# Kernel optimization log

Measured on AMD Instinct MI355X. Metric: run time of the kernel, lower is better.

## Reference

```python
import jax, jax.numpy as jnp
import numpy as np

B, C, IC, H = 16, 256, 64, 56
EPS = 1e-5
SCALE = float((H * H * C) ** -0.5)


def conv1x1(x, w, b=None):
    # x: [B,Cin,H,W], w: [Cout,Cin]
    y = jnp.einsum('bchw,oc->bohw', x, w)
    return y if b is None else y + b[None, :, None, None]


def bn_eval(x, g, be):
    # eval-mode BatchNorm2d with running_mean=0, running_var=1
    s = g / np.float32(np.sqrt(1.0 + EPS))
    return x * s[None, :, None, None] + be[None, :, None, None]


def lrelu(x):
    return jnp.where(x >= 0, x, 0.2 * x)


def setup_inputs() -> dict:
    key = jax.random.key(0)
    ks = jax.random.split(key, 16)
    def w(i, shape, s=0.05):
        return jax.random.normal(ks[i], shape, jnp.float32) * s
    return {
        'x_s': w(0, (B, C, H, H), 1.0),
        'x_fq': w(1, (B, C, H, H), 1.0),
        'x_mt': w(2, (B, C, H, H), 1.0),
        # local_att: conv(C->IC)+BN+LReLU+conv(IC->C)+BN
        'la_w1': w(3, (IC, C)), 'la_b1': jnp.zeros(IC, jnp.float32),
        'la_g1': jnp.ones(IC, jnp.float32), 'la_be1': jnp.zeros(IC, jnp.float32),
        'la_w2': w(4, (C, IC)), 'la_b2': jnp.zeros(C, jnp.float32),
        'la_g2': jnp.ones(C, jnp.float32), 'la_be2': jnp.zeros(C, jnp.float32),
        'lk_w': w(5, (C, C)), 'lk_b': jnp.zeros(C, jnp.float32),
        'lv_w': w(6, (C, C)),  # l_convv has bias=False
        # global_att (after avg-pool): conv+BN+LReLU+conv+BN
        'ga_w1': w(7, (IC, C)), 'ga_b1': jnp.zeros(IC, jnp.float32),
        'ga_g1': jnp.ones(IC, jnp.float32), 'ga_be1': jnp.zeros(IC, jnp.float32),
        'ga_w2': w(8, (C, IC)), 'ga_b2': jnp.zeros(C, jnp.float32),
        'ga_g2': jnp.ones(C, jnp.float32), 'ga_be2': jnp.zeros(C, jnp.float32),
        'gk_w': w(9, (C, C)), 'gk_b': jnp.zeros(C, jnp.float32),
        'gv_w': w(10, (C, C)),  # convv has bias=False
        'c11_w': w(11, (C, C)), 'c11_b': jnp.zeros(C, jnp.float32),
        'c1_w': w(12, (C, C)), 'c1_b': jnp.zeros(C, jnp.float32),
    }


def reference(x_s, x_fq, x_mt,
              la_w1, la_b1, la_g1, la_be1, la_w2, la_b2, la_g2, la_be2,
              lk_w, lk_b, lv_w,
              ga_w1, ga_b1, ga_g1, ga_be1, ga_w2, ga_b2, ga_g2, ga_be2,
              gk_w, gk_b, gv_w, c11_w, c11_b, c1_w, c1_b):
    # ---- local branch ----
    l_q = bn_eval(conv1x1(lrelu(bn_eval(conv1x1(x_s, la_w1, la_b1), la_g1, la_be1)),
                          la_w2, la_b2), la_g2, la_be2)
    l_k = conv1x1(x_s, lk_w, lk_b)
    l_v = conv1x1(x_s, lv_w)
    # l_q @ l_k^T over the spatial matrix of each (b,c): [H,W]@[W,H]->[H,H]
    att = jax.nn.softmax(jnp.einsum('bchw,bcvw->bchv', l_q, l_k) * SCALE, axis=-1)
    l_fuse = jnp.einsum('bchv,bcvw->bchw', att, l_v)  # [B,C,H,W]
    # ---- global branch ----
    p = jnp.mean(conv1x1(x_mt, c11_w, c11_b), axis=(2, 3), keepdims=True)  # [B,C,1,1]
    g_q = bn_eval(conv1x1(lrelu(bn_eval(conv1x1(p, ga_w1, ga_b1), ga_g1, ga_be1)),
                          ga_w2, ga_b2), ga_g2, ga_be2)  # [B,C,1,1]
    g_k = conv1x1(x_fq, gk_w, gk_b)
    g_v = conv1x1(x_fq, gv_w)
    gatt = jax.nn.softmax(g_q * g_k * SCALE, axis=-1)  # softmax over W
    g_fuse = jnp.einsum('bchk,bckw->bchw', gatt, g_v)  # requires H==W (square maps)
    # ---- output conv: kernel 1 with padding 1 -> spatial grows to H+2 ----
    f = jnp.pad(l_fuse + g_fuse, ((0, 0), (0, 0), (1, 1), (1, 1)))
    return conv1x1(f, c1_w, c1_b)  # [B,C,H+2,W+2]
```

## Files before the change

kernel.cpp:

```cpp
#include <hip/hip_runtime.h>
#include <hip/hip_bf16.h>

typedef __bf16 bf16;
typedef __bf16 bf16x8 __attribute__((ext_vector_type(8)));
typedef float  f32x4  __attribute__((ext_vector_type(4)));

#define S_SP 3136
#define SCALE_V (1.0f/896.0f)

__device__ __forceinline__ float bf2f(bf16 x) { return (float)x; }

__device__ __forceinline__ bf16x8 load8(const float* p) {
    f32x4 a = *(const f32x4*)p;
    f32x4 b = *(const f32x4*)(p + 4);
    bf16x8 r;
    r[0] = (bf16)a[0]; r[1] = (bf16)a[1]; r[2] = (bf16)a[2]; r[3] = (bf16)a[3];
    r[4] = (bf16)b[0]; r[5] = (bf16)b[1]; r[6] = (bf16)b[2]; r[7] = (bf16)b[3];
    return r;
}
__device__ __forceinline__ bf16x8 load8(const bf16* p) { return *(const bf16x8*)p; }

__global__ __launch_bounds__(256)
void conv_multi_kernel(const float* __restrict__ X,
                       const float* __restrict__ Wa, const float* __restrict__ ba,
                       bf16* __restrict__ Ya,
                       const float* __restrict__ Wb, bf16* __restrict__ Yb,
                       const float* __restrict__ Wc, const float* __restrict__ bc,
                       const float* __restrict__ gc, const float* __restrict__ bec,
                       bf16* __restrict__ Yc)
{
    __shared__ bf16 Xt[64][72];
    const int s0  = blockIdx.x * 64;
    const int sec = blockIdx.y;
    const int b   = blockIdx.z;
    const int tid = threadIdx.x;
    const int wv = tid >> 6, lane = tid & 63, li = lane & 15, quad = lane >> 4;

    const float* Xb = X + (size_t)b * 256 * S_SP;

    const float* W; const float* bias = nullptr;
    const float* bng = nullptr; const float* bnb = nullptr;
    bf16* Y; int o0, O; bool two, lrelu = false;
    if (sec < 2)      { W = Wa; bias = ba; Y = Ya; o0 = sec * 128;       two = true;  O = 256; }
    else if (sec < 4) { W = Wb;            Y = Yb; o0 = (sec - 2) * 128; two = true;  O = 256; }
    else              { W = Wc; bias = bc; bng = gc; bnb = bec; Y = Yc;
                        o0 = 0; two = false; lrelu = true; O = 64; }

    f32x4 acc[2][4];
    #pragma unroll
    for (int mt = 0; mt < 2; ++mt)
        #pragma unroll
        for (int nt = 0; nt < 4; ++nt) acc[mt][nt] = f32x4{0.f, 0.f, 0.f, 0.f};

    #pragma unroll
    for (int k0 = 0; k0 < 256; k0 += 32) {
        if (k0) __syncthreads();
        {
            int cl  = tid >> 3;
            int sj  = (tid & 7) * 8;
            int g   = cl >> 3;
            int clo = cl & 7;
            bf16x8 v = load8(Xb + (size_t)(k0 + cl) * S_SP + s0 + sj);
            #pragma unroll
            for (int u = 0; u < 8; ++u) {
                int r  = sj + u;
                int gp = g ^ ((r >> 3) & 3);
                Xt[r][gp * 8 + clo] = v[u];
            }
        }
        __syncthreads();
        bf16x8 a0 = load8(W + (size_t)(o0 + wv * 16 + li) * 256 + k0 + quad * 8);
        bf16x8 a1;
        if (two) a1 = load8(W + (size_t)(o0 + 64 + wv * 16 + li) * 256 + k0 + quad * 8);
        #pragma unroll
        for (int nt = 0; nt < 4; ++nt) {
            int row = nt * 16 + li;
            int gp  = quad ^ ((row >> 3) & 3);
            bf16x8 bb = *(const bf16x8*)&Xt[row][gp * 8];
            acc[0][nt] = __builtin_amdgcn_mfma_f32_16x16x32_bf16(a0, bb, acc[0][nt], 0, 0, 0);
            if (two)
                acc[1][nt] = __builtin_amdgcn_mfma_f32_16x16x32_bf16(a1, bb, acc[1][nt], 0, 0, 0);
        }
    }

    const float rs = rsqrtf(1.0f + 1e-5f);
    const int nm = two ? 2 : 1;
    for (int mt = 0; mt < nm; ++mt) {
        #pragma unroll
        for (int r = 0; r < 4; ++r) {
            int o = o0 + mt * 64 + wv * 16 + quad * 4 + r;
            float bi = bias ? bias[o] : 0.f;
            float sc = bng ? bng[o] * rs : 1.f;
            float sh = bnb ? bnb[o] : 0.f;
            #pragma unroll
            for (int nt = 0; nt < 4; ++nt) {
                float v = acc[mt][nt][r] + bi;
                v = v * sc + sh;
                if (lrelu) v = (v >= 0.f) ? v : 0.2f * v;
                int s = s0 + nt * 16 + li;
                Y[((size_t)b * O + o) * S_SP + s] = (bf16)v;
            }
        }
    }
}

template<typename TX, typename TY, int CIN, int MT, bool LRELU, bool PAD_OUT>
__global__ __launch_bounds__(256)
void conv1x1_kernel(const TX* __restrict__ X, const float* __restrict__ W,
                    const float* __restrict__ bias, const float* __restrict__ bng,
                    const float* __restrict__ bnb, TY* __restrict__ Y, int O)
{
    __shared__ bf16 Xt[64][72];
    const int s0  = blockIdx.x * 64;
    const int o0  = blockIdx.y * (MT * 64);
    const int b   = blockIdx.z;
    const int tid = threadIdx.x;
    const int wv = tid >> 6, lane = tid & 63, li = lane & 15, quad = lane >> 4;

    const TX* Xb = X + (size_t)b * CIN * S_SP;

    f32x4 acc[MT][4];
    #pragma unroll
    for (int mt = 0; mt < MT; ++mt)
        #pragma unroll
        for (int nt = 0; nt < 4; ++nt) acc[mt][nt] = f32x4{0.f, 0.f, 0.f, 0.f};

    #pragma unroll
    for (int k0 = 0; k0 < CIN; k0 += 32) {
        if (k0) __syncthreads();
        {
            int cl  = tid >> 3;
            int sj  = (tid & 7) * 8;
            int g   = cl >> 3;
            int clo = cl & 7;
            bf16x8 v = load8(Xb + (size_t)(k0 + cl) * S_SP + s0 + sj);
            #pragma unroll
            for (int u = 0; u < 8; ++u) {
                int r  = sj + u;
                int gp = g ^ ((r >> 3) & 3);
                Xt[r][gp * 8 + clo] = v[u];
            }
        }
        __syncthreads();
        bf16x8 a[MT];
        #pragma unroll
        for (int mt = 0; mt < MT; ++mt)
            a[mt] = load8(W + (size_t)(o0 + mt * 64 + wv * 16 + li) * CIN + k0 + quad * 8);
        #pragma unroll
        for (int nt = 0; nt < 4; ++nt) {
            int row = nt * 16 + li;
            int gp  = quad ^ ((row >> 3) & 3);
            bf16x8 bb = *(const bf16x8*)&Xt[row][gp * 8];
            #pragma unroll
            for (int mt = 0; mt < MT; ++mt)
                acc[mt][nt] = __builtin_amdgcn_mfma_f32_16x16x32_bf16(a[mt], bb, acc[mt][nt], 0, 0, 0);
        }
    }

    const float rs = rsqrtf(1.0f + 1e-5f);
    #pragma unroll
    for (int mt = 0; mt < MT; ++mt) {
        #pragma unroll
        for (int r = 0; r < 4; ++r) {
            int o = o0 + mt * 64 + wv * 16 + quad * 4 + r;
            float bi = bias ? bias[o] : 0.f;
            float sc = bng ? bng[o] * rs : 1.f;
            float sh = bnb ? bnb[o] : 0.f;
            #pragma unroll
            for (int nt = 0; nt < 4; ++nt) {
                float v = acc[mt][nt][r] + bi;
                v = v * sc + sh;
                if (LRELU) v = (v >= 0.f) ? v : 0.2f * v;
                int s = s0 + nt * 16 + li;
                if (!PAD_OUT) {
                    Y[((size_t)b * O + o) * S_SP + s] = (TY)v;
                } else {
                    int rr = s / 56, cc = s % 56;
                    Y[(((size_t)b * O + o) * 58 + rr + 1) * 58 + cc + 1] = (TY)v;
                }
            }
        }
    }
}

__global__ __launch_bounds__(256)
void attn_kernel(const bf16* __restrict__ Q, const bf16* __restrict__ K,
                 const bf16* __restrict__ V, const float* __restrict__ gq,
                 const bf16* __restrict__ GK, const bf16* __restrict__ GV,
                 bf16* __restrict__ F)
{
    __shared__ bf16 Qs[64][72], Ks[64][72], Vt[64][72], Ps[64][72];
    const int bc  = blockIdx.x;
    const int tid = threadIdx.x;
    const int wv = tid >> 6, lane = tid & 63, li = lane & 15, quad = lane >> 4;
    const int m0 = wv * 16;

    #pragma unroll
    for (int i = tid; i < 64 * 36; i += 256) {
        ((uint32_t*)Qs)[i] = 0; ((uint32_t*)Ks)[i] = 0;
        ((uint32_t*)Vt)[i] = 0; ((uint32_t*)Ps)[i] = 0;
    }
    __syncthreads();

    const bf16* Qp = Q + (size_t)bc * S_SP;
    const bf16* Kp = K + (size_t)bc * S_SP;
    const bf16* Vp = V + (size_t)bc * S_SP;
    for (int idx = tid; idx < 392; idx += 256) {
        int r = idx / 7, cj = (idx % 7) * 8;
        *(bf16x8*)&Qs[r][cj] = *(const bf16x8*)(Qp + r * 56 + cj);
        *(bf16x8*)&Ks[r][cj] = *(const bf16x8*)(Kp + r * 56 + cj);
        bf16x8 vv = *(const bf16x8*)(Vp + r * 56 + cj);
        int q = r >> 3, rlo = r & 7;
        #pragma unroll
        for (int u = 0; u < 8; ++u) {
            int row = cj + u;
            int gp  = q ^ ((row >> 3) & 3);
            Vt[row][gp * 8 + rlo] = vv[u];
        }
    }

    const float gs = gq[bc];
    const bf16* GVp = GV + (size_t)bc * S_SP;
    const bf16* GKp = GK + (size_t)bc * S_SP;
    const int ra  = tid / 7,            cja = (tid % 7) * 8;
    const bool hasb = tid < 136;
    const int rb  = (tid + 256) / 7,    cjb = ((tid + 256) % 7) * 8;
    bf16x8 gva = *(const bf16x8*)(GVp + ra * 56 + cja);
    bf16x8 gvb = hasb ? *(const bf16x8*)(GVp + rb * 56 + cjb) : bf16x8{};
    __syncthreads();

    f32x4 sacc[4];
    #pragma unroll
    for (int nt = 0; nt < 4; ++nt) sacc[nt] = f32x4{0.f, 0.f, 0.f, 0.f};
    #pragma unroll
    for (int k0 = 0; k0 < 64; k0 += 32) {
        bf16x8 a = *(const bf16x8*)&Qs[m0 + li][k0 + quad * 8];
        #pragma unroll
        for (int nt = 0; nt < 4; ++nt) {
            bf16x8 bb = *(const bf16x8*)&Ks[nt * 16 + li][k0 + quad * 8];
            sacc[nt] = __builtin_amdgcn_mfma_f32_16x16x32_bf16(a, bb, sacc[nt], 0, 0, 0);
        }
    }

    #pragma unroll
    for (int r = 0; r < 4; ++r) {
        float e[4]; float m = -3e38f;
        #pragma unroll
        for (int nt = 0; nt < 4; ++nt) {
            int v = nt * 16 + li;
            float x = (v < 56) ? sacc[nt][r] * SCALE_V : -3e38f;
            e[nt] = x; m = fmaxf(m, x);
        }
        m = fmaxf(m, __shfl_xor(m, 1)); m = fmaxf(m, __shfl_xor(m, 2));
        m = fmaxf(m, __shfl_xor(m, 4)); m = fmaxf(m, __shfl_xor(m, 8));
        float s = 0.f;
        #pragma unroll
        for (int nt = 0; nt < 4; ++nt) {
            float p = (nt * 16 + li < 56) ? __expf(e[nt] - m) : 0.f;
            e[nt] = p; s += p;
        }
        s += __shfl_xor(s, 1); s += __shfl_xor(s, 2);
        s += __shfl_xor(s, 4); s += __shfl_xor(s, 8);
        float inv = 1.f / s;
        int row = m0 + quad * 4 + r;
        #pragma unroll
        for (int nt = 0; nt < 4; ++nt) Ps[row][nt * 16 + li] = (bf16)(e[nt] * inv);
    }

    float gkv[4][4];
    #pragma unroll
    for (int r = 0; r < 4; ++r) {
        int row = m0 + quad * 4 + r;
        int hrow = (row < 56) ? row : 0;
        #pragma unroll
        for (int nt = 0; nt < 4; ++nt) {
            int v = nt * 16 + li;
            gkv[r][nt] = (v < 56) ? bf2f(GKp[hrow * 56 + v]) : 0.f;
        }
    }
    __syncthreads();

    f32x4 oacc[4];
    #pragma unroll
    for (int nt = 0; nt < 4; ++nt) oacc[nt] = f32x4{0.f, 0.f, 0.f, 0.f};
    #pragma unroll
    for (int k0 = 0; k0 < 64; k0 += 32) {
        bf16x8 a = *(const bf16x8*)&Ps[m0 + li][k0 + quad * 8];
        int kq = (k0 >> 3) + quad;
        #pragma unroll
        for (int nt = 0; nt < 4; ++nt) {
            int row = nt * 16 + li;
            int gp  = kq ^ ((row >> 3) & 3);
            bf16x8 bb = *(const bf16x8*)&Vt[row][gp * 8];
            oacc[nt] = __builtin_amdgcn_mfma_f32_16x16x32_bf16(a, bb, oacc[nt], 0, 0, 0);
        }
    }

    __syncthreads();

    {
        int q = ra >> 3, rlo = ra & 7;
        #pragma unroll
        for (int u = 0; u < 8; ++u) {
            int row = cja + u;
            int gp  = q ^ ((row >> 3) & 3);
            Vt[row][gp * 8 + rlo] = gva[u];
        }
        if (hasb) {
            int qb = rb >> 3, rblo = rb & 7;
            #pragma unroll
            for (int u = 0; u < 8; ++u) {
                int row = cjb + u;
                int gp  = qb ^ ((row >> 3) & 3);
                Vt[row][gp * 8 + rblo] = gvb[u];
            }
        }
    }

    #pragma unroll
    for (int r = 0; r < 4; ++r) {
        float e[4]; float m = -3e38f;
        #pragma unroll
        for (int nt = 0; nt < 4; ++nt) {
            int v = nt * 16 + li;
            float x = (v < 56) ? gs * gkv[r][nt] : -3e38f;
            e[nt] = x; m = fmaxf(m, x);
        }
        m = fmaxf(m, __shfl_xor(m, 1)); m = fmaxf(m, __shfl_xor(m, 2));
        m = fmaxf(m, __shfl_xor(m, 4)); m = fmaxf(m, __shfl_xor(m, 8));
        float s = 0.f;
        #pragma unroll
        for (int nt = 0; nt < 4; ++nt) {
            float p = (nt * 16 + li < 56) ? __expf(e[nt] - m) : 0.f;
            e[nt] = p; s += p;
        }
        s += __shfl_xor(s, 1); s += __shfl_xor(s, 2);
        s += __shfl_xor(s, 4); s += __shfl_xor(s, 8);
        float inv = 1.f / s;
        int row = m0 + quad * 4 + r;
        #pragma unroll
        for (int nt = 0; nt < 4; ++nt) Ps[row][nt * 16 + li] = (bf16)(e[nt] * inv);
    }
    __syncthreads();

    #pragma unroll
    for (int k0 = 0; k0 < 64; k0 += 32) {
        bf16x8 a = *(const bf16x8*)&Ps[m0 + li][k0 + quad * 8];
        int kq = (k0 >> 3) + quad;
        #pragma unroll
        for (int nt = 0; nt < 4; ++nt) {
            int row = nt * 16 + li;
            int gp  = kq ^ ((row >> 3) & 3);
            bf16x8 bb = *(const bf16x8*)&Vt[row][gp * 8];
            oacc[nt] = __builtin_amdgcn_mfma_f32_16x16x32_bf16(a, bb, oacc[nt], 0, 0, 0);
        }
    }

    bf16* Fp = F + (size_t)bc * S_SP;
    #pragma unroll
    for (int r = 0; r < 4; ++r) {
        int h = m0 + quad * 4 + r;
        #pragma unroll
        for (int nt = 0; nt < 4; ++nt) {
            int w = nt * 16 + li;
            if (h < 56 && w < 56) Fp[h * 56 + w] = (bf16)oacc[nt][r];
        }
    }
}

__global__ __launch_bounds__(256)
void spatial_mean_kernel(const float* __restrict__ X, float* __restrict__ out)
{
    int bc = blockIdx.x, tid = threadIdx.x;
    const float* p = X + (size_t)bc * S_SP;
    float s = 0.f;
    for (int i = tid; i < S_SP; i += 256) s += p[i];
    for (int off = 32; off; off >>= 1) s += __shfl_down(s, off, 64);
    __shared__ float ws[4];
    if ((tid & 63) == 0) ws[tid >> 6] = s;
    __syncthreads();
    if (tid == 0) out[bc] = (ws[0] + ws[1] + ws[2] + ws[3]) * (1.0f / S_SP);
}

__global__ __launch_bounds__(256)
void gq_kernel(const float* __restrict__ pmean,
               const float* c11w, const float* c11b,
               const float* gaw1, const float* gab1, const float* gag1, const float* gabe1,
               const float* gaw2, const float* gab2, const float* gag2, const float* gabe2,
               float* __restrict__ gq)
{
    __shared__ float pm[256], p2[256], hh[64];
    int b = blockIdx.x, t = threadIdx.x;
    pm[t] = pmean[b * 256 + t];
    __syncthreads();
    float a = c11b[t];
    for (int c = 0; c < 256; ++c) a += c11w[t * 256 + c] * pm[c];
    p2[t] = a;
    __syncthreads();
    const float rs = rsqrtf(1.0f + 1e-5f);
    if (t < 64) {
        float h = gab1[t];
        for (int c = 0; c < 256; ++c) h += gaw1[t * 256 + c] * p2[c];
        h = h * (gag1[t] * rs) + gabe1[t];
        hh[t] = (h >= 0.f) ? h : 0.2f * h;
    }
    __syncthreads();
    float g = gab2[t];
    for (int i = 0; i < 64; ++i) g += gaw2[t * 64 + i] * hh[i];
    g = g * (gag2[t] * rs) + gabe2[t];
    gq[b * 256 + t] = g * SCALE_V;
}

__global__ __launch_bounds__(256)
void fill_border_kernel(float* __restrict__ out, const float* __restrict__ c1b)
{
    int idx = blockIdx.x * 256 + threadIdx.x;
    int e  = idx % 228;
    int bo = idx / 228;
    if (bo >= 16 * 256) return;
    int o = bo & 255;
    int r, c;
    if (e < 58)       { r = 0;  c = e; }
    else if (e < 116) { r = 57; c = e - 58; }
    else { int t = e - 116; r = 1 + (t >> 1); c = (t & 1) * 57; }
    out[(size_t)bo * 3364 + r * 58 + c] = c1b[o];
}

extern "C" void kernel_launch(void* const* d_in, const int* in_sizes, int n_in,
                              void* d_out, int out_size, void* d_ws, size_t ws_size,
                              hipStream_t stream)
{
    (void)in_sizes; (void)n_in; (void)out_size; (void)ws_size;
    const float* x_s   = (const float*)d_in[0];
    const float* x_fq  = (const float*)d_in[1];
    const float* x_mt  = (const float*)d_in[2];
    const float* la_w1 = (const float*)d_in[3];
    const float* la_b1 = (const float*)d_in[4];
    const float* la_g1 = (const float*)d_in[5];
    const float* la_be1= (const float*)d_in[6];
    const float* la_w2 = (const float*)d_in[7];
    const float* la_b2 = (const float*)d_in[8];
    const float* la_g2 = (const float*)d_in[9];
    const float* la_be2= (const float*)d_in[10];
    const float* lk_w  = (const float*)d_in[11];
    const float* lk_b  = (const float*)d_in[12];
    const float* lv_w  = (const float*)d_in[13];
    const float* ga_w1 = (const float*)d_in[14];
    const float* ga_b1 = (const float*)d_in[15];
    const float* ga_g1 = (const float*)d_in[16];
    const float* ga_be1= (const float*)d_in[17];
    const float* ga_w2 = (const float*)d_in[18];
    const float* ga_b2 = (const float*)d_in[19];
    const float* ga_g2 = (const float*)d_in[20];
    const float* ga_be2= (const float*)d_in[21];
    const float* gk_w  = (const float*)d_in[22];
    const float* gk_b  = (const float*)d_in[23];
    const float* gv_w  = (const float*)d_in[24];
    const float* c11_w = (const float*)d_in[25];
    const float* c11_b = (const float*)d_in[26];
    const float* c1_w  = (const float*)d_in[27];
    const float* c1_b  = (const float*)d_in[28];
    float* out = (float*)d_out;

    char* ws = (char*)d_ws;
    const size_t SZ = (size_t)16 * 256 * S_SP * 2;
    bf16* Q  = (bf16*)(ws);
    bf16* K  = (bf16*)(ws + SZ);
    bf16* V  = (bf16*)(ws + 2 * SZ);
    bf16* GK = (bf16*)(ws + 3 * SZ);
    bf16* GV = (bf16*)(ws + 4 * SZ);
    bf16* Hd = (bf16*)(ws + 5 * SZ);
    float* pmean = (float*)(ws + 5 * SZ + (size_t)16 * 64 * S_SP * 2);
    float* gq    = pmean + 16 * 256;
    bf16* F  = Q;

    dim3 blk(256);
    fill_border_kernel<<<dim3(3648), blk, 0, stream>>>(out, c1_b);

    conv_multi_kernel<<<dim3(49, 5, 16), blk, 0, stream>>>(
        x_s, lk_w, lk_b, K, lv_w, V,
        la_w1, la_b1, la_g1, la_be1, Hd);
    conv1x1_kernel<bf16, bf16, 64, 2, false, false><<<dim3(49, 2, 16), blk, 0, stream>>>(
        Hd, la_w2, la_b2, la_g2, la_be2, Q, 256);

    spatial_mean_kernel<<<dim3(4096), blk, 0, stream>>>(x_mt, pmean);
    gq_kernel<<<dim3(16), blk, 0, stream>>>(pmean, c11_w, c11_b,
        ga_w1, ga_b1, ga_g1, ga_be1, ga_w2, ga_b2, ga_g2, ga_be2, gq);
    conv_multi_kernel<<<dim3(49, 4, 16), blk, 0, stream>>>(
        x_fq, gk_w, gk_b, GK, gv_w, GV,
        nullptr, nullptr, nullptr, nullptr, nullptr);

    attn_kernel<<<dim3(4096), blk, 0, stream>>>(Q, K, V, gq, GK, GV, F);

    conv1x1_kernel<bf16, float, 256, 2, false, true><<<dim3(49, 2, 16), blk, 0, stream>>>(
        F, c1_w, c1_b, nullptr, nullptr, out, 256);
}
```

Baseline: 508.4 us.

## Double-buffer conv input tiles and remap workgroups so XCDs share input tiles

```diff
diff --git a/kernel.cpp b/kernel.cpp
--- a/kernel.cpp
+++ b/kernel.cpp
@@ -20,6 +20,21 @@
 }
 __device__ __forceinline__ bf16x8 load8(const bf16* p) { return *(const bf16x8*)p; }
 
+template<typename T> struct raw8;
+template<> struct raw8<float> { f32x4 a, b; };
+template<> struct raw8<bf16>  { bf16x8 v; };
+__device__ __forceinline__ raw8<float> loadraw(const float* p) {
+    return { *(const f32x4*)p, *(const f32x4*)(p + 4) };
+}
+__device__ __forceinline__ raw8<bf16> loadraw(const bf16* p) {
+    return { *(const bf16x8*)p };
+}
+__device__ __forceinline__ bf16 elem8(const raw8<float>& r, int u) {
+    return (bf16)(u < 4 ? r.a[u] : r.b[u - 4]);
+}
+__device__ __forceinline__ bf16 elem8(const raw8<bf16>& r, int u) { return r.v[u]; }
+
+template<int NSEC>
 __global__ __launch_bounds__(256)
 void conv_multi_kernel(const float* __restrict__ X,
                        const float* __restrict__ Wa, const float* __restrict__ ba,
@@ -29,10 +44,15 @@
                        const float* __restrict__ gc, const float* __restrict__ bec,
                        bf16* __restrict__ Yc)
 {
-    __shared__ bf16 Xt[64][72];
-    const int s0  = blockIdx.x * 64;
-    const int sec = blockIdx.y;
-    const int b   = blockIdx.z;
+    __shared__ bf16 Xt[2][64][72];
+    const int wg  = blockIdx.x;
+    const int xcd = wg & 7;
+    const int idx = wg >> 3;
+    const int sec = idx % NSEC;
+    const int t   = idx / NSEC;
+    const int tile = xcd * 98 + t;
+    const int s0  = (tile % 49) * 64;
+    const int b   = tile / 49;
     const int tid = threadIdx.x;
     const int wv = tid >> 6, lane = tid & 63, li = lane & 15, quad = lane >> 4;
 
@@ -52,22 +72,24 @@
         #pragma unroll
         for (int nt = 0; nt < 4; ++nt) acc[mt][nt] = f32x4{0.f, 0.f, 0.f, 0.f};
 
+    const int cl  = tid >> 3;
+    const int sj  = (tid & 7) * 8;
+    const int g   = cl >> 3;
+    const int clo = cl & 7;
+    const float* xp = Xb + (size_t)cl * S_SP + s0 + sj;
+
+    raw8<float> v = loadraw(xp);
+    int p = 0;
     #pragma unroll
     for (int k0 = 0; k0 < 256; k0 += 32) {
-        if (k0) __syncthreads();
-        {
-            int cl  = tid >> 3;
-            int sj  = (tid & 7) * 8;
-            int g   = cl >> 3;
-            int clo = cl & 7;
-            bf16x8 v = load8(Xb + (size_t)(k0 + cl) * S_SP + s0 + sj);
-            #pragma unroll
-            for (int u = 0; u < 8; ++u) {
-                int r  = sj + u;
-                int gp = g ^ ((r >> 3) & 3);
-                Xt[r][gp * 8 + clo] = v[u];
-            }
-        }
+        #pragma unroll
+        for (int u = 0; u < 8; ++u) {
+            int r  = sj + u;
+            int gp = g ^ ((r >> 3) & 3);
+            Xt[p][r][gp * 8 + clo] = elem8(v, u);
+        }
+        raw8<float> vn = v;
+        if (k0 + 32 < 256) vn = loadraw(xp + (size_t)(k0 + 32) * S_SP);
         __syncthreads();
         bf16x8 a0 = load8(W + (size_t)(o0 + wv * 16 + li) * 256 + k0 + quad * 8);
         bf16x8 a1;
@@ -76,11 +98,13 @@
         for (int nt = 0; nt < 4; ++nt) {
             int row = nt * 16 + li;
             int gp  = quad ^ ((row >> 3) & 3);
-            bf16x8 bb = *(const bf16x8*)&Xt[row][gp * 8];
+            bf16x8 bb = *(const bf16x8*)&Xt[p][row][gp * 8];
             acc[0][nt] = __builtin_amdgcn_mfma_f32_16x16x32_bf16(a0, bb, acc[0][nt], 0, 0, 0);
             if (two)
                 acc[1][nt] = __builtin_amdgcn_mfma_f32_16x16x32_bf16(a1, bb, acc[1][nt], 0, 0, 0);
         }
+        v = vn;
+        p ^= 1;
     }
 
     const float rs = rsqrtf(1.0f + 1e-5f);
@@ -94,26 +118,32 @@
             float sh = bnb ? bnb[o] : 0.f;
             #pragma unroll
             for (int nt = 0; nt < 4; ++nt) {
-                float v = acc[mt][nt][r] + bi;
-                v = v * sc + sh;
-                if (lrelu) v = (v >= 0.f) ? v : 0.2f * v;
+                float val = acc[mt][nt][r] + bi;
+                val = val * sc + sh;
+                if (lrelu) val = (val >= 0.f) ? val : 0.2f * val;
                 int s = s0 + nt * 16 + li;
-                Y[((size_t)b * O + o) * S_SP + s] = (bf16)v;
+                Y[((size_t)b * O + o) * S_SP + s] = (bf16)val;
             }
         }
     }
 }
 
-template<typename TX, typename TY, int CIN, int MT, bool LRELU, bool PAD_OUT>
+template<typename TX, typename TY, int CIN, int MT, int NSEC, bool LRELU, bool PAD_OUT>
 __global__ __launch_bounds__(256)
 void conv1x1_kernel(const TX* __restrict__ X, const float* __restrict__ W,
                     const float* __restrict__ bias, const float* __restrict__ bng,
                     const float* __restrict__ bnb, TY* __restrict__ Y, int O)
 {
-    __shared__ bf16 Xt[64][72];
-    const int s0  = blockIdx.x * 64;
-    const int o0  = blockIdx.y * (MT * 64);
-    const int b   = blockIdx.z;
+    __shared__ bf16 Xt[2][64][72];
+    const int wg  = blockIdx.x;
+    const int xcd = wg & 7;
+    const int idx = wg >> 3;
+    const int sec = idx % NSEC;
+    const int t   = idx / NSEC;
+    const int tile = xcd * 98 + t;
+    const int s0  = (tile % 49) * 64;
+    const int b   = tile / 49;
+    const int o0  = sec * (MT * 64);
     const int tid = threadIdx.x;
     const int wv = tid >> 6, lane = tid & 63, li = lane & 15, quad = lane >> 4;
 
@@ -125,22 +155,24 @@
         #pragma unroll
         for (int nt = 0; nt < 4; ++nt) acc[mt][nt] = f32x4{0.f, 0.f, 0.f, 0.f};
 
+    const int cl  = tid >> 3;
+    const int sj  = (tid & 7) * 8;
+    const int g   = cl >> 3;
+    const int clo = cl & 7;
+    const TX* xp = Xb + (size_t)cl * S_SP + s0 + sj;
+
+    raw8<TX> v = loadraw(xp);
+    int p = 0;
     #pragma unroll
     for (int k0 = 0; k0 < CIN; k0 += 32) {
-        if (k0) __syncthreads();
-        {
-            int cl  = tid >> 3;
-            int sj  = (tid & 7) * 8;
-            int g   = cl >> 3;
-            int clo = cl & 7;
-            bf16x8 v = load8(Xb + (size_t)(k0 + cl) * S_SP + s0 + sj);
-            #pragma unroll
-            for (int u = 0; u < 8; ++u) {
-                int r  = sj + u;
-                int gp = g ^ ((r >> 3) & 3);
-                Xt[r][gp * 8 + clo] = v[u];
-            }
-        }
+        #pragma unroll
+        for (int u = 0; u < 8; ++u) {
+            int r  = sj + u;
+            int gp = g ^ ((r >> 3) & 3);
+            Xt[p][r][gp * 8 + clo] = elem8(v, u);
+        }
+        raw8<TX> vn = v;
+        if (k0 + 32 < CIN) vn = loadraw(xp + (size_t)(k0 + 32) * S_SP);
         __syncthreads();
         bf16x8 a[MT];
         #pragma unroll
@@ -150,11 +182,13 @@
         for (int nt = 0; nt < 4; ++nt) {
             int row = nt * 16 + li;
             int gp  = quad ^ ((row >> 3) & 3);
-            bf16x8 bb = *(const bf16x8*)&Xt[row][gp * 8];
+            bf16x8 bb = *(const bf16x8*)&Xt[p][row][gp * 8];
             #pragma unroll
             for (int mt = 0; mt < MT; ++mt)
                 acc[mt][nt] = __builtin_amdgcn_mfma_f32_16x16x32_bf16(a[mt], bb, acc[mt][nt], 0, 0, 0);
         }
+        v = vn;
+        p ^= 1;
     }
 
     const float rs = rsqrtf(1.0f + 1e-5f);
@@ -168,15 +202,15 @@
             float sh = bnb ? bnb[o] : 0.f;
             #pragma unroll
             for (int nt = 0; nt < 4; ++nt) {
-                float v = acc[mt][nt][r] + bi;
-                v = v * sc + sh;
-                if (LRELU) v = (v >= 0.f) ? v : 0.2f * v;
+                float val = acc[mt][nt][r] + bi;
+                val = val * sc + sh;
+                if (LRELU) val = (val >= 0.f) ? val : 0.2f * val;
                 int s = s0 + nt * 16 + li;
                 if (!PAD_OUT) {
-                    Y[((size_t)b * O + o) * S_SP + s] = (TY)v;
+                    Y[((size_t)b * O + o) * S_SP + s] = (TY)val;
                 } else {
                     int rr = s / 56, cc = s % 56;
-                    Y[(((size_t)b * O + o) * 58 + rr + 1) * 58 + cc + 1] = (TY)v;
+                    Y[(((size_t)b * O + o) * 58 + rr + 1) * 58 + cc + 1] = (TY)val;
                 }
             }
         }
@@ -256,8 +290,8 @@
         float s = 0.f;
         #pragma unroll
         for (int nt = 0; nt < 4; ++nt) {
-            float p = (nt * 16 + li < 56) ? __expf(e[nt] - m) : 0.f;
-            e[nt] = p; s += p;
+            float pp = (nt * 16 + li < 56) ? __expf(e[nt] - m) : 0.f;
+            e[nt] = pp; s += pp;
         }
         s += __shfl_xor(s, 1); s += __shfl_xor(s, 2);
         s += __shfl_xor(s, 4); s += __shfl_xor(s, 8);
@@ -331,8 +365,8 @@
         float s = 0.f;
         #pragma unroll
         for (int nt = 0; nt < 4; ++nt) {
-            float p = (nt * 16 + li < 56) ? __expf(e[nt] - m) : 0.f;
-            e[nt] = p; s += p;
+            float pp = (nt * 16 + li < 56) ? __expf(e[nt] - m) : 0.f;
+            e[nt] = pp; s += pp;
         }
         s += __shfl_xor(s, 1); s += __shfl_xor(s, 2);
         s += __shfl_xor(s, 4); s += __shfl_xor(s, 8);
@@ -477,21 +511,21 @@
     dim3 blk(256);
     fill_border_kernel<<<dim3(3648), blk, 0, stream>>>(out, c1_b);
 
-    conv_multi_kernel<<<dim3(49, 5, 16), blk, 0, stream>>>(
+    conv_multi_kernel<5><<<dim3(8 * 98 * 5), blk, 0, stream>>>(
         x_s, lk_w, lk_b, K, lv_w, V,
         la_w1, la_b1, la_g1, la_be1, Hd);
-    conv1x1_kernel<bf16, bf16, 64, 2, false, false><<<dim3(49, 2, 16), blk, 0, stream>>>(
+    conv1x1_kernel<bf16, bf16, 64, 2, 2, false, false><<<dim3(8 * 98 * 2), blk, 0, stream>>>(
         Hd, la_w2, la_b2, la_g2, la_be2, Q, 256);
 
     spatial_mean_kernel<<<dim3(4096), blk, 0, stream>>>(x_mt, pmean);
     gq_kernel<<<dim3(16), blk, 0, stream>>>(pmean, c11_w, c11_b,
         ga_w1, ga_b1, ga_g1, ga_be1, ga_w2, ga_b2, ga_g2, ga_be2, gq);
-    conv_multi_kernel<<<dim3(49, 4, 16), blk, 0, stream>>>(
+    conv_multi_kernel<4><<<dim3(8 * 98 * 4), blk, 0, stream>>>(
         x_fq, gk_w, gk_b, GK, gv_w, GV,
         nullptr, nullptr, nullptr, nullptr, nullptr);
 
     attn_kernel<<<dim3(4096), blk, 0, stream>>>(Q, K, V, gq, GK, GV, F);
 
-    conv1x1_kernel<bf16, float, 256, 2, false, true><<<dim3(49, 2, 16), blk, 0, stream>>>(
+    conv1x1_kernel<bf16, float, 256, 2, 2, false, true><<<dim3(8 * 98 * 2), blk, 0, stream>>>(
         F, c1_w, c1_b, nullptr, nullptr, out, 256);
 }
```

After: 497.0 us. -2.2%, faster.
